# Optimization experiments

Measured on AMD Instinct MI355X. Metric: run time of the kernel, lower is better.

## Reference

```python
import jax, jax.numpy as jnp
import numpy as np
import math

B, S, DIN, E, H, WIN = 2, 2048, 512, 512, 8, 256
HD = E // H


def setup_inputs() -> dict:
    key = jax.random.key(0)
    k0, k1, k2, k3 = jax.random.split(key, 4)
    x = jax.random.normal(k0, (B, S, DIN), jnp.float32)
    padding_mask = jax.random.randint(k1, (B, S), 0, 2).astype(jnp.int32)
    # xavier-ish scale so attention logits are reasonable
    w_qkv = jax.random.normal(k2, (3 * E, DIN), jnp.float32) * (1.0 / math.sqrt(DIN))
    b_qkv = jnp.zeros((3 * E,), jnp.float32)
    w_o = jax.random.normal(k3, (E, E), jnp.float32) * (1.0 / math.sqrt(E))
    b_o = jnp.zeros((E,), jnp.float32)
    return {"x": x, "padding_mask": padding_mask, "w_qkv": w_qkv, "b_qkv": b_qkv,
            "w_o": w_o, "b_o": b_o}


def reference(x, padding_mask, w_qkv, b_qkv, w_o, b_o):
    b, s, _ = x.shape
    qkv = x @ w_qkv.T + b_qkv                     # [B,S,3E]
    qkv = qkv.reshape(b, s, H, 3 * HD).transpose(0, 2, 1, 3)  # [B,H,S,3hd]
    q, k, v = jnp.split(qkv, 3, axis=-1)          # each [B,H,S,hd]

    scale = 1.0 / math.sqrt(HD)                   # function scales by sqrt(head_dim)
    scores = jnp.einsum('bhqd,bhkd->bhqk', q, k) * scale  # [B,H,S,S]

    # Torch ref scatter_adds windowed scores into a zeros(S,S) matrix; zero-padded
    # keys contribute exactly 0 at clamped indices, so this equals band-masking.
    i = jnp.arange(s)[:, None]
    j = jnp.arange(s)[None, :]
    band = jnp.abs(i - j) <= WIN // 2             # [S,S]
    scores = jnp.where(band, scores, 0.0)
    # torch: atten_scores[atten_scores == 0.0] = -inf (kills off-band and exact zeros)
    scores = jnp.where(scores == 0.0, -jnp.inf, scores)
    # torch detaches the scores before softmax
    scores = jax.lax.stop_gradient(scores)

    key_mask = padding_mask[:, None, None, :] == 0    # [B,1,1,S]
    qry_mask = padding_mask[:, None, :, None] == 0    # [B,1,S,1]
    scores = jnp.where(key_mask, -jnp.inf, scores)
    scores = jnp.where(qry_mask, -jnp.inf, scores)

    attn = jax.nn.softmax(scores, axis=-1)
    attn = jnp.where(jnp.isnan(attn), 0.0, attn)   # fully-masked rows -> 0

    vals = jnp.einsum('bhqk,bhkd->bhqd', attn, v)  # [B,H,S,hd]
    vals = vals.transpose(0, 2, 1, 3).reshape(b, s, E)
    return vals @ w_o.T + b_o


if __name__ == '__main__':
    out = reference(**setup_inputs())
    print(out.shape)
```

## Files before the change

### kernel.cpp

```cpp
#include <hip/hip_runtime.h>
#include <math.h>

#define B 2
#define S 2048
#define H 8
#define HD 64
#define E 512
#define N3E 1536
#define M 4096
#define HALF 128

typedef unsigned short u16;
typedef unsigned int u32;
using short8 = __attribute__((ext_vector_type(8))) short;
using f32x4  = __attribute__((ext_vector_type(4))) float;

__device__ __forceinline__ u32 bfhi(float v) {
    union { float f; u32 u; } c; c.f = v;
    return (c.u + 0x7fffu + ((c.u >> 16) & 1u)) >> 16;
}
__device__ __forceinline__ float bff(u32 b) {
    union { u32 u; float f; } c; c.u = b << 16; return c.f;
}


__global__ __launch_bounds__(256) void prep_all(
    const float* __restrict__ x,    u16* __restrict__ XAh,
    const float* __restrict__ wqkv, u16* __restrict__ WBh,
    const float* __restrict__ wo,   u16* __restrict__ OBh)
{
    const int wv = threadIdx.x >> 6, ln = threadIdx.x & 63;
    const float* src; u16* dh; int Ti;
    if (blockIdx.x < 1024)      { src = x;    dh = XAh; Ti = blockIdx.x * 4 + wv; }
    else if (blockIdx.x < 1408) { src = wqkv; dh = WBh; Ti = (blockIdx.x - 1024) * 4 + wv; }
    else                        { src = wo;   dh = OBh; Ti = (blockIdx.x - 1408) * 4 + wv; }

    const int rt = Ti >> 4, kb = Ti & 15;
    const int row = rt * 16 + (ln & 15);
    const int kc  = kb * 32 + (ln >> 4) * 8;
    const float4* s = (const float4*)(src + (size_t)row * 512 + kc);
    float4 v0 = s[0], v1 = s[1];
    float f[8] = {v0.x, v0.y, v0.z, v0.w, v1.x, v1.y, v1.z, v1.w};
    short8 hs;
    #pragma unroll
    for (int e = 0; e < 8; ++e) hs[e] = (short)bfhi(f[e]);
    *(short8*)(dh + (size_t)Ti * 512 + ln * 8) = hs;
}

__global__ __launch_bounds__(256) void qkv_mfma(
    const u16* __restrict__ XAh, const u16* __restrict__ WBh,
    const float* __restrict__ bias, const int* __restrict__ mask,
    u16* __restrict__ QF, u16* __restrict__ KF, u16* __restrict__ VB)
{
    const int lin = blockIdx.x;
    const int c = lin & 7, rest = lin >> 3;
    const int bx = rest & 15;
    const int by = (rest >> 4) * 8 + c;

    const int wv = threadIdx.x >> 6, ln = threadIdx.x & 63;
    const int waveM = wv >> 1, waveN = wv & 1;
    const int mtb = by * 8 + waveM * 4;
    const int ntb = bx * 6 + waveN * 3;
    const int lr = ln & 15, lk = ln >> 4;

    f32x4 acc[4][3] = {};

    for (int kb = 0; kb < 16; ++kb) {
        short8 a_h[4], b_h[3];
        #pragma unroll
        for (int i = 0; i < 4; ++i)
            a_h[i] = *(const short8*)(XAh + ((size_t)(mtb + i) * 16 + kb) * 512 + ln * 8);
        #pragma unroll
        for (int j = 0; j < 3; ++j)
            b_h[j] = *(const short8*)(WBh + ((size_t)(ntb + j) * 16 + kb) * 512 + ln * 8);
        #pragma unroll
        for (int i = 0; i < 4; ++i)
            #pragma unroll
            for (int j = 0; j < 3; ++j)
                acc[i][j] = __builtin_amdgcn_mfma_f32_16x16x32_bf16(a_h[i], b_h[j], acc[i][j], 0, 0, 0);
    }

    int rmask[4][4];
    #pragma unroll
    for (int i = 0; i < 4; ++i) {
        const int mb = (mtb + i) * 16 + lk * 4;
        #pragma unroll
        for (int r = 0; r < 4; ++r) rmask[i][r] = mask[mb + r];
    }

    #pragma unroll
    for (int j = 0; j < 3; ++j) {
        const int n  = (ntb + j) * 16 + lr;
        const int h  = n / 192;
        const int rr = n % 192;
        const int wh = rr >> 6;
        const int d  = rr & 63;
        const float bv = bias[n];
        #pragma unroll
        for (int i = 0; i < 4; ++i) {
            const int mbase = (mtb + i) * 16 + lk * 4;
            const int b_ = mbase >> 11;
            const int s0 = mbase & 2047;
            const int bh = b_ * 8 + h;
            u32 hb[4];
            #pragma unroll
            for (int r = 0; r < 4; ++r) {
                float val = acc[i][j][r] + bv;
                if (wh < 2 && rmask[i][r] == 0) val = 0.f;
                hb[r] = bfhi(val);
            }
            if (wh < 2) {
                const int dh_  = d >> 5;
                const int kgrp = (d & 31) >> 3;
                const int jj   = d & 7;
                const int tt   = s0 >> 4;
                const int lane0 = kgrp * 16 + lk * 4;
                u16* dst = (wh == 0) ? QF : KF;
                const size_t basea =
                    (((size_t)bh * 128 + tt) * 2 + dh_) * 512 + jj;
                #pragma unroll
                for (int r = 0; r < 4; ++r)
                    dst[basea + (size_t)(lane0 + r) * 8] = (u16)hb[r];
            } else {
                const int st  = s0 >> 5;
                const int dt  = d >> 4;
                const int sb0 = s0 & 31;
                const int lane_v = ((sb0 >> 3) << 4) | (d & 15);
                const int j0  = sb0 & 7;
                short4 h4;
                h4.x = (short)hb[0]; h4.y = (short)hb[1];
                h4.z = (short)hb[2]; h4.w = (short)hb[3];
                *(short4*)(VB + (((size_t)bh * 64 + st) * 4 + dt) * 512
                              + lane_v * 8 + j0) = h4;
            }
        }
    }
}

__global__ __launch_bounds__(512, 8) void attn_mfma(
    const u16* __restrict__ QF, const u16* __restrict__ KF,
    const u16* __restrict__ VB, u16* __restrict__ VF)
{
    __shared__ u16   scb[32 * 296];
    __shared__ float rowsum[32];

    const int tid = threadIdx.x;
    const int wv = tid >> 6, ln = tid & 63;
    const int lr = ln & 15, lk = ln >> 4;
    const int bh = blockIdx.x & 15;
    const int i0 = (blockIdx.x >> 4) * 32;

    const int klo = max(0, i0 - HALF);
    const int khi = min(S - 1, i0 + 31 + HALF);
    const int kcount = khi - klo + 1;
    const int nkt = kcount >> 4, nks = kcount >> 5;
    const int kt0 = klo >> 4, st0 = klo >> 5;

    if (tid < 32) rowsum[tid] = 0.f;
    __syncthreads();

    const int mi = wv >> 2;

    short8 qa_h[2];
    {
        const int qt = (i0 >> 4) + mi;
        #pragma unroll
        for (int dh = 0; dh < 2; ++dh)
            qa_h[dh] = *(const short8*)(QF + (((size_t)bh * 128 + qt) * 2 + dh) * 512 + ln * 8);
    }

    float psum[4] = {0.f, 0.f, 0.f, 0.f};
    for (int ni = (wv & 3); ni < nkt; ni += 4) {
        const int key = klo + ni * 16 + lr;
        f32x4 acc = {};
        #pragma unroll
        for (int dh = 0; dh < 2; ++dh) {
            short8 kh_ = *(const short8*)(KF + (((size_t)bh * 128 + kt0 + ni) * 2 + dh) * 512 + ln * 8);
            acc = __builtin_amdgcn_mfma_f32_16x16x32_bf16(qa_h[dh], kh_, acc, 0, 0, 0);
        }
        #pragma unroll
        for (int r = 0; r < 4; ++r) {
            const int row = mi * 16 + lk * 4 + r;
            const int qr  = i0 + row;
            float s = acc[r] * 0.125f;
            const bool valid = ((u32)(key - qr + HALF) <= 2 * HALF) && (s != 0.0f);
            float p = valid ? __expf(s) : 0.f;
            u32 pb = bfhi(p);
            scb[row * 296 + ni * 16 + lr] = (u16)pb;
            psum[r] += bff(pb);
        }
    }
    #pragma unroll
    for (int off = 1; off <= 8; off <<= 1)
        #pragma unroll
        for (int r = 0; r < 4; ++r)
            psum[r] += __shfl_xor(psum[r], off);
    if (lr == 0) {
        #pragma unroll
        for (int r = 0; r < 4; ++r)
            atomicAdd(&rowsum[mi * 16 + lk * 4 + r], psum[r]);
    }
    __syncthreads();

    const int dt = wv & 3;
    f32x4 acc2 = {};
    for (int ks = 0; ks < nks; ++ks) {
        short8 pa = *(const short8*)&scb[(mi * 16 + lr) * 296 + ks * 32 + lk * 8];
        short8 vh = *(const short8*)(VB + (((size_t)bh * 64 + st0 + ks) * 4 + dt) * 512 + ln * 8);
        acc2 = __builtin_amdgcn_mfma_f32_16x16x32_bf16(pa, vh, acc2, 0, 0, 0);
    }

    const int b = bh >> 3, h = bh & 7;
    #pragma unroll
    for (int r = 0; r < 4; ++r) {
        const int row = mi * 16 + lk * 4 + r;
        const float rs = rowsum[row];
        const float inv = (rs > 0.f) ? 1.f / rs : 0.f;
        const int m = b * S + i0 + row;
        const int mt = m >> 4, lrm = m & 15;
        const int e = h * 64 + dt * 16 + lr;
        const int kb = e >> 5, rem = e & 31;
        VF[((size_t)(mt * 16 + kb) * 64 + (rem >> 3) * 16 + lrm) * 8 + (rem & 7)]
            = (u16)bfhi(acc2[r] * inv);
    }
}

__global__ __launch_bounds__(256) void outproj_mfma(
    const u16* __restrict__ VF, const u16* __restrict__ OBh,
    const float* __restrict__ bo, float* __restrict__ out)
{
    const int lin = blockIdx.x;
    const int c = lin & 7, rest = lin >> 3;
    const int bx = rest & 7;
    const int by = (rest >> 3) * 8 + c;

    const int wv = threadIdx.x >> 6, ln = threadIdx.x & 63;
    const int waveM = wv >> 1, waveN = wv & 1;
    const int mtb = by * 8 + waveM * 4;
    const int ntb = bx * 4 + waveN * 2;
    const int lr = ln & 15, lk = ln >> 4;

    f32x4 acc[4][2] = {};

    for (int kb = 0; kb < 16; ++kb) {
        short8 a[4], b_h[2];
        #pragma unroll
        for (int i = 0; i < 4; ++i)
            a[i] = *(const short8*)(VF + ((size_t)(mtb + i) * 16 + kb) * 512 + ln * 8);
        #pragma unroll
        for (int j = 0; j < 2; ++j)
            b_h[j] = *(const short8*)(OBh + ((size_t)(ntb + j) * 16 + kb) * 512 + ln * 8);
        #pragma unroll
        for (int i = 0; i < 4; ++i)
            #pragma unroll
            for (int j = 0; j < 2; ++j)
                acc[i][j] = __builtin_amdgcn_mfma_f32_16x16x32_bf16(a[i], b_h[j], acc[i][j], 0, 0, 0);
    }

    #pragma unroll
    for (int j = 0; j < 2; ++j) {
        const int n = (ntb + j) * 16 + lr;
        const float bv = bo[n];
        #pragma unroll
        for (int i = 0; i < 4; ++i)
            #pragma unroll
            for (int r = 0; r < 4; ++r) {
                const int m = (mtb + i) * 16 + lk * 4 + r;
                out[(size_t)m * 512 + n] = acc[i][j][r] + bv;
            }
    }
}

extern "C" void kernel_launch(void* const* d_in, const int* in_sizes, int n_in,
                              void* d_out, int out_size, void* d_ws, size_t ws_size,
                              hipStream_t stream)
{
    const float* x     = (const float*)d_in[0];
    const int*   pmask = (const int*)d_in[1];
    const float* w_qkv = (const float*)d_in[2];
    const float* b_qkv = (const float*)d_in[3];
    const float* w_o   = (const float*)d_in[4];
    const float* b_o   = (const float*)d_in[5];
    float* out = (float*)d_out;

    u16* XAh = (u16*)d_out;

    char* w8 = (char*)d_ws;
    u16* WBh = (u16*)(w8 + 0);
    u16* OBh = (u16*)(w8 + 3145728);
    u16* QF  = (u16*)(w8 + 4194304);
    u16* KF  = (u16*)(w8 + 12582912);
    u16* VB  = (u16*)(w8 + 20971520);
    u16* VF  = (u16*)(w8 + 29360128);

    prep_all<<<1536, 256, 0, stream>>>(x, XAh, w_qkv, WBh, w_o, OBh);
    qkv_mfma<<<512, 256, 0, stream>>>(XAh, WBh, b_qkv, pmask, QF, KF, VB);
    attn_mfma<<<1024, 512, 0, stream>>>(QF, KF, VB, VF);
    outproj_mfma<<<256, 256, 0, stream>>>(VF, OBh, b_o, out);
}
```

Before: 109.5 us.

## Stage QKV GEMM tiles in LDS with double buffering; share K tiles across query rows

The QKV projection kernel now copies each k-step's A and B tiles into double-buffered shared memory using direct global-to-LDS loads. Each wave then reads its fragments from LDS instead of each wave re-reading overlapping tiles from global memory. In the attention kernel, each wave now loads a key tile once and computes scores for both 16-row query tiles with it, striding over key tiles by 8 instead of 4, which halves redundant K loads. The cost is an extra barrier per k-step and more registers for the second Q fragment and accumulator.

```diff
diff --git a/kernel.cpp b/kernel.cpp
--- a/kernel.cpp
+++ b/kernel.cpp
@@ -23,6 +23,12 @@
     union { u32 u; float f; } c; c.u = b << 16; return c.f;
 }
 
+__device__ __forceinline__ void stage16(const u16* g, u16* l) {
+    __builtin_amdgcn_global_load_lds(
+        (const __attribute__((address_space(1))) void*)g,
+        (__attribute__((address_space(3))) void*)l, 16, 0, 0);
+}
+
 
 __global__ __launch_bounds__(256) void prep_all(
     const float* __restrict__ x,    u16* __restrict__ XAh,
@@ -52,6 +58,9 @@
     const float* __restrict__ bias, const int* __restrict__ mask,
     u16* __restrict__ QF, u16* __restrict__ KF, u16* __restrict__ VB)
 {
+    __shared__ u16 sA[2][8 * 512];
+    __shared__ u16 sB[2][6 * 512];
+
     const int lin = blockIdx.x;
     const int c = lin & 7, rest = lin >> 3;
     const int bx = rest & 15;
@@ -59,26 +68,52 @@
 
     const int wv = threadIdx.x >> 6, ln = threadIdx.x & 63;
     const int waveM = wv >> 1, waveN = wv & 1;
-    const int mtb = by * 8 + waveM * 4;
-    const int ntb = bx * 6 + waveN * 3;
+    const int mtb0 = by * 8, ntb0 = bx * 6;
+    const int mtb = mtb0 + waveM * 4;
+    const int ntb = ntb0 + waveN * 3;
     const int lr = ln & 15, lk = ln >> 4;
 
     f32x4 acc[4][3] = {};
 
+#define STAGE_QKV(buf, kbi) do {                                             \
+        if (wv < 2) {                                                        \
+            _Pragma("unroll")                                                \
+            for (int t = 0; t < 4; ++t) {                                    \
+                const int tt = wv * 4 + t;                                   \
+                stage16(XAh + ((size_t)(mtb0 + tt) * 16 + (kbi)) * 512 + ln * 8, \
+                        &sA[buf][tt * 512]);                                 \
+            }                                                                \
+        } else {                                                             \
+            _Pragma("unroll")                                                \
+            for (int t = 0; t < 3; ++t) {                                    \
+                const int tt = (wv - 2) * 3 + t;                             \
+                stage16(WBh + ((size_t)(ntb0 + tt) * 16 + (kbi)) * 512 + ln * 8, \
+                        &sB[buf][tt * 512]);                                 \
+            }                                                                \
+        }                                                                    \
+    } while (0)
+
+    STAGE_QKV(0, 0);
+
     for (int kb = 0; kb < 16; ++kb) {
+        const int cur = kb & 1;
+        __syncthreads();
+        if (kb + 1 < 16) STAGE_QKV(cur ^ 1, kb + 1);
+
         short8 a_h[4], b_h[3];
         #pragma unroll
         for (int i = 0; i < 4; ++i)
-            a_h[i] = *(const short8*)(XAh + ((size_t)(mtb + i) * 16 + kb) * 512 + ln * 8);
+            a_h[i] = *(const short8*)&sA[cur][(waveM * 4 + i) * 512 + ln * 8];
         #pragma unroll
         for (int j = 0; j < 3; ++j)
-            b_h[j] = *(const short8*)(WBh + ((size_t)(ntb + j) * 16 + kb) * 512 + ln * 8);
+            b_h[j] = *(const short8*)&sB[cur][(waveN * 3 + j) * 512 + ln * 8];
         #pragma unroll
         for (int i = 0; i < 4; ++i)
             #pragma unroll
             for (int j = 0; j < 3; ++j)
                 acc[i][j] = __builtin_amdgcn_mfma_f32_16x16x32_bf16(a_h[i], b_h[j], acc[i][j], 0, 0, 0);
     }
+#undef STAGE_QKV
 
     int rmask[4][4];
     #pragma unroll
@@ -159,49 +194,58 @@
     if (tid < 32) rowsum[tid] = 0.f;
     __syncthreads();
 
+    short8 qa_h[2][2];
+    {
+        const int qt0 = i0 >> 4;
+        #pragma unroll
+        for (int m2 = 0; m2 < 2; ++m2)
+            #pragma unroll
+            for (int dh = 0; dh < 2; ++dh)
+                qa_h[m2][dh] = *(const short8*)(QF + (((size_t)bh * 128 + qt0 + m2) * 2 + dh) * 512 + ln * 8);
+    }
+
+    float psum[2][4] = {};
+    for (int ni = wv; ni < nkt; ni += 8) {
+        const int key = klo + ni * 16 + lr;
+        short8 kh0 = *(const short8*)(KF + (((size_t)bh * 128 + kt0 + ni) * 2 + 0) * 512 + ln * 8);
+        short8 kh1 = *(const short8*)(KF + (((size_t)bh * 128 + kt0 + ni) * 2 + 1) * 512 + ln * 8);
+        f32x4 acc0 = {}, acc1 = {};
+        acc0 = __builtin_amdgcn_mfma_f32_16x16x32_bf16(qa_h[0][0], kh0, acc0, 0, 0, 0);
+        acc0 = __builtin_amdgcn_mfma_f32_16x16x32_bf16(qa_h[0][1], kh1, acc0, 0, 0, 0);
+        acc1 = __builtin_amdgcn_mfma_f32_16x16x32_bf16(qa_h[1][0], kh0, acc1, 0, 0, 0);
+        acc1 = __builtin_amdgcn_mfma_f32_16x16x32_bf16(qa_h[1][1], kh1, acc1, 0, 0, 0);
+        #pragma unroll
+        for (int m2 = 0; m2 < 2; ++m2) {
+            #pragma unroll
+            for (int r = 0; r < 4; ++r) {
+                const int row = m2 * 16 + lk * 4 + r;
+                const int qr  = i0 + row;
+                float s = (m2 ? acc1[r] : acc0[r]) * 0.125f;
+                const bool valid = ((u32)(key - qr + HALF) <= 2 * HALF) && (s != 0.0f);
+                float p = valid ? __expf(s) : 0.f;
+                u32 pb = bfhi(p);
+                scb[row * 296 + ni * 16 + lr] = (u16)pb;
+                psum[m2][r] += bff(pb);
+            }
+        }
+    }
+    #pragma unroll
+    for (int off = 1; off <= 8; off <<= 1)
+        #pragma unroll
+        for (int m2 = 0; m2 < 2; ++m2)
+            #pragma unroll
+            for (int r = 0; r < 4; ++r)
+                psum[m2][r] += __shfl_xor(psum[m2][r], off);
+    if (lr == 0) {
+        #pragma unroll
+        for (int m2 = 0; m2 < 2; ++m2)
+            #pragma unroll
+            for (int r = 0; r < 4; ++r)
+                atomicAdd(&rowsum[m2 * 16 + lk * 4 + r], psum[m2][r]);
+    }
+    __syncthreads();
+
     const int mi = wv >> 2;
-
-    short8 qa_h[2];
-    {
-        const int qt = (i0 >> 4) + mi;
-        #pragma unroll
-        for (int dh = 0; dh < 2; ++dh)
-            qa_h[dh] = *(const short8*)(QF + (((size_t)bh * 128 + qt) * 2 + dh) * 512 + ln * 8);
-    }
-
-    float psum[4] = {0.f, 0.f, 0.f, 0.f};
-    for (int ni = (wv & 3); ni < nkt; ni += 4) {
-        const int key = klo + ni * 16 + lr;
-        f32x4 acc = {};
-        #pragma unroll
-        for (int dh = 0; dh < 2; ++dh) {
-            short8 kh_ = *(const short8*)(KF + (((size_t)bh * 128 + kt0 + ni) * 2 + dh) * 512 + ln * 8);
-            acc = __builtin_amdgcn_mfma_f32_16x16x32_bf16(qa_h[dh], kh_, acc, 0, 0, 0);
-        }
-        #pragma unroll
-        for (int r = 0; r < 4; ++r) {
-            const int row = mi * 16 + lk * 4 + r;
-            const int qr  = i0 + row;
-            float s = acc[r] * 0.125f;
-            const bool valid = ((u32)(key - qr + HALF) <= 2 * HALF) && (s != 0.0f);
-            float p = valid ? __expf(s) : 0.f;
-            u32 pb = bfhi(p);
-            scb[row * 296 + ni * 16 + lr] = (u16)pb;
-            psum[r] += bff(pb);
-        }
-    }
-    #pragma unroll
-    for (int off = 1; off <= 8; off <<= 1)
-        #pragma unroll
-        for (int r = 0; r < 4; ++r)
-            psum[r] += __shfl_xor(psum[r], off);
-    if (lr == 0) {
-        #pragma unroll
-        for (int r = 0; r < 4; ++r)
-            atomicAdd(&rowsum[mi * 16 + lk * 4 + r], psum[r]);
-    }
-    __syncthreads();
-
     const int dt = wv & 3;
     f32x4 acc2 = {};
     for (int ks = 0; ks < nks; ++ks) {
```

Result: no change. 109.3 us (-0.2%).
